# Optimization experiments

Measured on AMD Instinct MI355X. Metric: run time of the kernel, lower is better.

The kernel has to match this reference:

```python
import jax, jax.numpy as jnp
import numpy as np

V, E, H, O, B, T = 50000, 128, 128, 128, 64, 512


def setup_inputs() -> dict:
    key = jax.random.key(0)
    ks = jax.random.split(key, 16)
    s = 0.05
    X = jax.random.randint(ks[0], (B, T), 0, V)
    lens = jnp.sort(jax.random.randint(ks[1], (B,), 64, T + 1))[::-1]
    lens = lens.at[0].set(T)  # pack_padded needs descending lengths, max == T
    emb = jax.random.normal(ks[2], (V, E)) * s
    emb = emb.at[0].set(0.0)  # padding_idx = 0
    return {
        "X": X,
        "X_lengths": lens,
        "batch_size": B,
        "emb": emb,
        "W_e2i": jax.random.normal(ks[3], (H, E)) * s,
        "b_e2i": jax.random.normal(ks[4], (H,)) * s,
        "Wih_f": jax.random.normal(ks[5], (3 * H, H)) * s,
        "Whh_f": jax.random.normal(ks[6], (3 * H, H)) * s,
        "bih_f": jax.random.normal(ks[7], (3 * H,)) * s,
        "bhh_f": jax.random.normal(ks[8], (3 * H,)) * s,
        "Wih_b": jax.random.normal(ks[9], (3 * H, H)) * s,
        "Whh_b": jax.random.normal(ks[10], (3 * H, H)) * s,
        "bih_b": jax.random.normal(ks[11], (3 * H,)) * s,
        "bhh_b": jax.random.normal(ks[12], (3 * H,)) * s,
        "W_h2o": jax.random.normal(ks[13], (O, 2 * H)) * s,
        "b_h2o": jax.random.normal(ks[14], (O,)) * s,
        "u_w": jax.random.uniform(ks[15], (O,)),  # torch.rand
    }


def _gru_scan(gx, mask_tb, Whh, bhh):
    """gx: [T,B,3H] precomputed input gates; mask_tb: [T,B,1] valid-step mask.
    Masked update emulates pack_padded_sequence: padded steps keep h unchanged
    (and h stays 0 before the first valid step of the reversed direction)."""
    h0 = jnp.zeros((gx.shape[1], Whh.shape[1]), gx.dtype)

    def step(h, tb):
        gxt, m = tb
        gh = h @ Whh.T + bhh
        gxr, gxz, gxn = jnp.split(gxt, 3, axis=-1)
        ghr, ghz, ghn = jnp.split(gh, 3, axis=-1)
        r = jax.nn.sigmoid(gxr + ghr)
        z = jax.nn.sigmoid(gxz + ghz)
        n = jnp.tanh(gxn + r * ghn)
        h_new = (1.0 - z) * n + z * h
        h = jnp.where(m, h_new, h)
        return h, h

    _, hs = jax.lax.scan(step, h0, (gx, mask_tb))
    return hs  # [T,B,H]


def reference(X, X_lengths, batch_size, emb, W_e2i, b_e2i,
              Wih_f, Whh_f, bih_f, bhh_f, Wih_b, Whh_b, bih_b, bhh_b,
              W_h2o, b_h2o, u_w):
    x = emb[X]                              # [B,T,E]
    x = x @ W_e2i.T + b_e2i                 # [B,T,H]
    Tn = x.shape[1]
    mask = jnp.arange(Tn)[None, :] < X_lengths[:, None]  # [B,T]
    m_tb = mask.T[:, :, None]               # [T,B,1]

    gx_f = (x @ Wih_f.T + bih_f).transpose(1, 0, 2)       # [T,B,3H]
    h_f = _gru_scan(gx_f, m_tb, Whh_f, bhh_f)             # [T,B,H]
    gx_b = (x @ Wih_b.T + bih_b).transpose(1, 0, 2)[::-1]
    h_b = _gru_scan(gx_b, m_tb[::-1], Whh_b, bhh_b)[::-1]

    Hout = jnp.concatenate([h_f, h_b], axis=-1).transpose(1, 0, 2)  # [B,T,2H]
    Hout = Hout * mask[:, :, None].astype(Hout.dtype)  # pad_packed zeros pads

    Y = jnp.tanh(Hout @ W_h2o.T + b_h2o)               # [B,T,O]
    scores = jnp.where(mask, (Y * u_w).sum(-1), -jnp.inf)  # [B,T]
    alpha = jax.nn.softmax(scores, axis=1)             # per-sample softmax over valid steps
    pooled = jnp.einsum("bt,btd->bd", alpha, Hout)     # [B,2H]
    return pooled[None]                                # [1,B,2H]
```

## Files before the change

kernel.cpp:

```cpp
#include <hip/hip_runtime.h>
#include <hip/hip_bf16.h>

#define VV 50000
#define EE 128
#define HH 128
#define OO 128
#define BB 64
#define TT 512

typedef __bf16 bf16_t;
typedef __attribute__((ext_vector_type(8))) __bf16 bf16x8;
typedef __attribute__((ext_vector_type(4))) __bf16 bf16x4;
typedef __attribute__((ext_vector_type(4))) float floatx4;

__device__ __forceinline__ bf16x8 ldb8(const bf16_t* p) {
    return *reinterpret_cast<const bf16x8*>(p);
}

__device__ __forceinline__ bf16x8 ldf8_bf(const float* p) {
    const float4* q = reinterpret_cast<const float4*>(p);
    float4 u = q[0], v = q[1];
    bf16x8 r;
    r[0] = (__bf16)u.x; r[1] = (__bf16)u.y; r[2] = (__bf16)u.z; r[3] = (__bf16)u.w;
    r[4] = (__bf16)v.x; r[5] = (__bf16)v.y; r[6] = (__bf16)v.z; r[7] = (__bf16)v.w;
    return r;
}

__device__ __forceinline__ float fast_rcp(float x) { return __builtin_amdgcn_rcpf(x); }
__device__ __forceinline__ float sigmoid_f(float x) {
    return fast_rcp(1.0f + __expf(-x));
}
__device__ __forceinline__ float tanh_f(float x) {
    float e = __expf(2.0f * x);
    return 1.0f - 2.0f * fast_rcp(e + 1.0f);
}

__device__ __forceinline__ void lds_barrier() {
    asm volatile("s_waitcnt lgkmcnt(0)\n\ts_barrier" ::: "memory");
}

__global__ __launch_bounds__(256) void k0_conv(
    const float* __restrict__ we,
    const float* __restrict__ wihf, const float* __restrict__ wihb,
    const float* __restrict__ whhf, const float* __restrict__ whhb,
    const float* __restrict__ wh2o,
    const float* __restrict__ bihf, const float* __restrict__ bhhf,
    const float* __restrict__ bihb, const float* __restrict__ bhhb,
    bf16_t* __restrict__ we_bf,
    bf16_t* __restrict__ wih_bf, bf16_t* __restrict__ whh_bf,
    bf16_t* __restrict__ wh2o_bf, float* __restrict__ gxbias) {
    int tid = blockIdx.x * 256 + threadIdx.x;
    int np = gridDim.x * 256;
    for (int i = tid; i < HH * EE; i += np) we_bf[i] = (bf16_t)we[i];
    for (int i = tid; i < 384 * HH; i += np) {
        wih_bf[i] = (bf16_t)wihf[i];
        wih_bf[384 * HH + i] = (bf16_t)wihb[i];
        whh_bf[i] = (bf16_t)whhf[i];
        whh_bf[384 * HH + i] = (bf16_t)whhb[i];
    }
    for (int i = tid; i < OO * 256; i += np) wh2o_bf[i] = (bf16_t)wh2o[i];
    if (tid < 768) {
        int dir = tid / 384, n = tid % 384;
        const float* bih = dir ? bihb : bihf;
        const float* bhh = dir ? bhhb : bhhf;
        gxbias[tid] = bih[n] + (n < 256 ? bhh[n] : 0.0f);
    }
}

__global__ __launch_bounds__(256) void k12_gx(const int* __restrict__ X,
                                              const float* __restrict__ emb,
                                              const bf16_t* __restrict__ we_bf,
                                              const float* __restrict__ be,
                                              const bf16_t* __restrict__ wih_bf,
                                              const float* __restrict__ gxbias,
                                              const int* __restrict__ lens,
                                              bf16_t* __restrict__ gx3) {
    int blk = blockIdx.x;
    int tq = blk >> 2;
    int g = blk & 3;
    if (4 * tq >= lens[16 * g]) return;

    int lane = threadIdx.x & 63;
    int w2 = threadIdx.x >> 6;
    int quad = lane >> 4, col = lane & 15;

    __shared__ bf16_t xs[4][16 * 136];

#pragma unroll
    for (int tt = 0; tt < 4; ++tt) {
        int t = 4 * tq + tt;
        int v = X[(g * 16 + col) * TT + t];
        bf16x8 a[4];
#pragma unroll
        for (int kc = 0; kc < 4; ++kc)
            a[kc] = ldf8_bf(emb + (size_t)v * EE + kc * 32 + quad * 8);
#pragma unroll
        for (int tl = 0; tl < 2; ++tl) {
            int n = 32 * w2 + 16 * tl + col;
            floatx4 acc = {0.f, 0.f, 0.f, 0.f};
#pragma unroll
            for (int kc = 0; kc < 4; ++kc) {
                bf16x8 bw = ldb8(we_bf + (size_t)n * EE + kc * 32 + quad * 8);
                acc = __builtin_amdgcn_mfma_f32_16x16x32_bf16(a[kc], bw, acc, 0, 0, 0);
            }
            float bias = be[n];
#pragma unroll
            for (int r = 0; r < 4; ++r)
                xs[tt][(quad * 4 + r) * 136 + n] = (bf16_t)(acc[r] + bias);
        }
    }
    __syncthreads();

    bf16x8 a2[4][4];
#pragma unroll
    for (int tt = 0; tt < 4; ++tt)
#pragma unroll
        for (int kc = 0; kc < 4; ++kc)
            a2[tt][kc] = ldb8(xs[tt] + col * 136 + kc * 32 + quad * 8);

#pragma unroll
    for (int tl = 0; tl < 12; ++tl) {
        int idx = w2 * 12 + tl;
        int dir = idx >= 24;
        int n = (idx - dir * 24) * 16 + col;
        bf16x8 bw[4];
#pragma unroll
        for (int kc = 0; kc < 4; ++kc)
            bw[kc] = ldb8(wih_bf + ((size_t)dir * 384 + n) * HH + kc * 32 + quad * 8);
        float bias = gxbias[dir * 384 + n];
#pragma unroll
        for (int tt = 0; tt < 4; ++tt) {
            int t = 4 * tq + tt;
            floatx4 acc = {0.f, 0.f, 0.f, 0.f};
#pragma unroll
            for (int kc = 0; kc < 4; ++kc)
                acc = __builtin_amdgcn_mfma_f32_16x16x32_bf16(a2[tt][kc], bw[kc], acc, 0, 0, 0);
            bf16x4 pack;
#pragma unroll
            for (int r = 0; r < 4; ++r)
                pack[r] = (__bf16)(acc[r] + bias);
            *reinterpret_cast<bf16x4*>(
                gx3 + (((size_t)(dir * 16 + 4 * g + quad) * TT + t) * 384 + n) * 4) = pack;
        }
    }
}

#define HPAD 144
#define HBUF (4 * HPAD)
__global__ __launch_bounds__(512) void k3_gru(const bf16_t* __restrict__ gx3,
                                              const bf16_t* __restrict__ whh_bf,
                                              const float* __restrict__ bhh_f,
                                              const float* __restrict__ bhh_b,
                                              const int* __restrict__ lens,
                                              bf16_t* __restrict__ hist2) {
    int g16 = blockIdx.x;
    int dir = blockIdx.y;
    const float* bhh = dir ? bhh_b : bhh_f;

    int tid = threadIdx.x;
    int w = tid >> 6;
    int lane = tid & 63;
    int quad = lane >> 4, col = lane & 15;
    int j = 16 * w + col;

    __shared__ bf16_t hl[2 * HBUF];
    for (int i = tid; i < 2 * HBUF; i += 512) hl[i] = (bf16_t)0.f;

    int len1 = lens[4 * g16 + quad];
    int Lmax = max(max(lens[4 * g16], lens[4 * g16 + 1]),
                   max(lens[4 * g16 + 2], lens[4 * g16 + 3]));

    float bhn = bhh[256 + j];

    bf16x8 Bw[3][4];
#pragma unroll
    for (int gate = 0; gate < 3; ++gate)
#pragma unroll
        for (int kc = 0; kc < 4; ++kc)
            Bw[gate][kc] = ldb8(whh_bf + ((size_t)dir * 384 + gate * 128 + j) * HH + kc * 32 + quad * 8);

    const bf16_t* gbase = gx3 + (size_t)(dir * 16 + g16) * TT * 1536;
    bf16_t* hb = hist2 + (size_t)(dir * 16 + g16) * TT * 512;
    int loff[3];
#pragma unroll
    for (int gate = 0; gate < 3; ++gate)
        loff[gate] = (gate * 128 + j) * 4 + quad;
    int hoff = quad * 128 + j;
    int aoff = (col & 3) * HPAD + quad * 8;

    float h = 0.f;
    int S4 = (Lmax + 3) & ~3;
    bool lowquad = (quad & 1) == 0;
    bool lowhalf = (quad & 2) == 0;

    __bf16 ring[4][3];
#pragma unroll
    for (int u = 0; u < 4; ++u) {
        int tr = dir ? (Lmax - 1 - u) : u;
        int t = min(max(tr, 0), Lmax - 1);
#pragma unroll
        for (int gate = 0; gate < 3; ++gate)
            ring[u][gate] = gbase[(size_t)t * 1536 + loff[gate]];
    }
    lds_barrier();

    for (int sb = 0; sb < S4; sb += 4) {
#pragma unroll
        for (int u = 0; u < 4; ++u) {
            int s = sb + u;
            int tr = dir ? (Lmax - 1 - s) : s;
            int t = min(max(tr, 0), Lmax - 1);
            const bf16_t* hc = hl + (s & 1) * HBUF;
            bf16_t* hn = hl + ((s + 1) & 1) * HBUF;

            float gx0 = (float)ring[u][0];
            float gx1 = (float)ring[u][1];
            float gx2 = (float)ring[u][2];

            bf16x8 a[4];
#pragma unroll
            for (int kc = 0; kc < 4; ++kc)
                a[kc] = ldb8(hc + aoff + kc * 32);

            floatx4 cr = {0.f, 0.f, 0.f, 0.f};
            floatx4 cz = {0.f, 0.f, 0.f, 0.f};
            floatx4 cn = {bhn, bhn, bhn, bhn};
#pragma unroll
            for (int kc = 0; kc < 4; ++kc) {
                cr = __builtin_amdgcn_mfma_f32_16x16x32_bf16(a[kc], Bw[0][kc], cr, 0, 0, 0);
                cz = __builtin_amdgcn_mfma_f32_16x16x32_bf16(a[kc], Bw[1][kc], cz, 0, 0, 0);
                cn = __builtin_amdgcn_mfma_f32_16x16x32_bf16(a[kc], Bw[2][kc], cn, 0, 0, 0);
            }

            {
                int sn = s + 4;
                int trn = dir ? (Lmax - 1 - sn) : sn;
                int tn = min(max(trn, 0), Lmax - 1);
#pragma unroll
                for (int gate = 0; gate < 3; ++gate)
                    ring[u][gate] = gbase[(size_t)tn * 1536 + loff[gate]];
            }

            float aR = lowhalf ? (lowquad ? cr[0] : cr[1]) : (lowquad ? cr[2] : cr[3]);
            float aZ = lowhalf ? (lowquad ? cz[0] : cz[1]) : (lowquad ? cz[2] : cz[3]);
            float aN = lowhalf ? (lowquad ? cn[0] : cn[1]) : (lowquad ? cn[2] : cn[3]);

            float rg = sigmoid_f(aR + gx0);
            float zg = sigmoid_f(aZ + gx1);
            float ng = tanh_f(gx2 + rg * aN);
            float hnew = ng + zg * (h - ng);
            bool upd = (s < Lmax) && (t < len1);
            h = upd ? hnew : h;
            bf16_t h16 = (bf16_t)h;
            hn[quad * HPAD + j] = h16;
            hb[(size_t)t * 512 + hoff] = h16;

            lds_barrier();
        }
    }
}

__global__ __launch_bounds__(256) void k45_pool(const bf16_t* __restrict__ hist2,
                                                const bf16_t* __restrict__ wh2o_bf,
                                                const float* __restrict__ bh2o,
                                                const float* __restrict__ uw,
                                                const int* __restrict__ lens,
                                                float* __restrict__ out) {
    int b = blockIdx.x;
    int g16 = b >> 2, bl = b & 3;
    int tid = threadIdx.x;
    int lane = tid & 63, w2 = tid >> 6;
    int quad = lane >> 4, col = lane & 15;
    int len = lens[b];

    __shared__ float smax[TT][4];
    __shared__ float alpha[TT];
    __shared__ float red[256];

    const bf16_t* hf = hist2 + (size_t)g16 * TT * 512 + bl * 128;
    const bf16_t* hbk = hist2 + (size_t)(16 + g16) * TT * 512 + bl * 128;

    int n0 = (w2 * 2 + 0) * 16 + col;
    int n1 = (w2 * 2 + 1) * 16 + col;
    float bias0 = bh2o[n0], u0 = uw[n0];
    float bias1 = bh2o[n1], u1 = uw[n1];

    int nch = (len + 15) >> 4;
    for (int ch = 0; ch < nch; ++ch) {
        int t0 = ch * 16;
        int t = t0 + col;
        bf16x8 a[8];
#pragma unroll
        for (int kc = 0; kc < 4; ++kc) {
            a[kc]     = ldb8(hf  + (size_t)t * 512 + kc * 32 + quad * 8);
            a[kc + 4] = ldb8(hbk + (size_t)t * 512 + kc * 32 + quad * 8);
        }
        float p4[4] = {0.f, 0.f, 0.f, 0.f};
#pragma unroll
        for (int tl = 0; tl < 2; ++tl) {
            int n = tl ? n1 : n0;
            float bias = tl ? bias1 : bias0;
            float u = tl ? u1 : u0;
            floatx4 acc = {0.f, 0.f, 0.f, 0.f};
#pragma unroll
            for (int kc = 0; kc < 8; ++kc) {
                bf16x8 bw = ldb8(wh2o_bf + (size_t)n * 256 + kc * 32 + quad * 8);
                acc = __builtin_amdgcn_mfma_f32_16x16x32_bf16(a[kc], bw, acc, 0, 0, 0);
            }
#pragma unroll
            for (int r = 0; r < 4; ++r)
                p4[r] += tanh_f(acc[r] + bias) * u;
        }
#pragma unroll
        for (int m = 1; m < 16; m <<= 1)
#pragma unroll
            for (int r = 0; r < 4; ++r)
                p4[r] += __shfl_xor(p4[r], m, 64);
        if (col == 0) {
#pragma unroll
            for (int r = 0; r < 4; ++r)
                smax[t0 + quad * 4 + r][w2] = p4[r];
        }
    }
    __syncthreads();

    float mx = -1e30f;
    for (int t = tid; t < TT; t += 256) {
        float s = -1e30f;
        if (t < len) s = smax[t][0] + smax[t][1] + smax[t][2] + smax[t][3];
        alpha[t] = s;
        mx = fmaxf(mx, s);
    }
    red[tid] = mx;
    __syncthreads();
    for (int s = 128; s > 0; s >>= 1) {
        if (tid < s) red[tid] = fmaxf(red[tid], red[tid + s]);
        __syncthreads();
    }
    mx = red[0];
    __syncthreads();
    float sum = 0.f;
    for (int t = tid; t < TT; t += 256) {
        float e = (t < len) ? __expf(alpha[t] - mx) : 0.f;
        alpha[t] = e;
        sum += e;
    }
    red[tid] = sum;
    __syncthreads();
    for (int s = 128; s > 0; s >>= 1) {
        if (tid < s) red[tid] += red[tid + s];
        __syncthreads();
    }
    float inv = fast_rcp(red[0]);
    __syncthreads();

    int c = tid;
    int dir = c >> 7;
    int j = c & 127;
    const bf16_t* hbase = (dir ? hbk : hf) + j;
    float acc = 0.f;
    int t = 0;
    for (; t + 4 <= len; t += 4) {
        acc += alpha[t + 0] * (float)hbase[(size_t)(t + 0) * 512];
        acc += alpha[t + 1] * (float)hbase[(size_t)(t + 1) * 512];
        acc += alpha[t + 2] * (float)hbase[(size_t)(t + 2) * 512];
        acc += alpha[t + 3] * (float)hbase[(size_t)(t + 3) * 512];
    }
    for (; t < len; ++t) acc += alpha[t] * (float)hbase[(size_t)t * 512];

    out[(size_t)b * 256 + c] = acc * inv;
}

extern "C" void kernel_launch(void* const* d_in, const int* in_sizes, int n_in,
                              void* d_out, int out_size, void* d_ws, size_t ws_size,
                              hipStream_t stream) {
    const int* X       = (const int*)d_in[0];
    const int* lens    = (const int*)d_in[1];
    const float* emb   = (const float*)d_in[3];
    const float* We2i  = (const float*)d_in[4];
    const float* be2i  = (const float*)d_in[5];
    const float* Wihf  = (const float*)d_in[6];
    const float* Whhf  = (const float*)d_in[7];
    const float* bihf  = (const float*)d_in[8];
    const float* bhhf  = (const float*)d_in[9];
    const float* Wihb  = (const float*)d_in[10];
    const float* Whhb  = (const float*)d_in[11];
    const float* bihb  = (const float*)d_in[12];
    const float* bhhb  = (const float*)d_in[13];
    const float* Wh2o  = (const float*)d_in[14];
    const float* bh2o  = (const float*)d_in[15];
    const float* uw    = (const float*)d_in[16];

    char* ws = (char*)d_ws;
    size_t off = 0;
    bf16_t* we_bf = (bf16_t*)(ws + off);   off += (size_t)HH * EE * 2;
    bf16_t* wih_bf = (bf16_t*)(ws + off);  off += (size_t)2 * 384 * HH * 2;
    bf16_t* whh_bf = (bf16_t*)(ws + off);  off += (size_t)2 * 384 * HH * 2;
    bf16_t* wh2o_bf = (bf16_t*)(ws + off); off += (size_t)OO * 256 * 2;
    float* gxbias = (float*)(ws + off);    off += 768 * 4;
    off = (off + 255) & ~(size_t)255;
    bf16_t* gx3 = (bf16_t*)(ws + off);     off += (size_t)32 * TT * 384 * 4 * 2;
    bf16_t* hist2 = (bf16_t*)(ws + off);   off += (size_t)32 * TT * 4 * 128 * 2;

    float* out = (float*)d_out;

    k0_conv<<<dim3(256), dim3(256), 0, stream>>>(We2i, Wihf, Wihb, Whhf, Whhb,
                                                 Wh2o, bihf, bhhf, bihb, bhhb,
                                                 we_bf, wih_bf, whh_bf, wh2o_bf, gxbias);
    k12_gx<<<dim3(TT), dim3(256), 0, stream>>>(X, emb, we_bf, be2i, wih_bf, gxbias, lens, gx3);
    k3_gru<<<dim3(16, 2), dim3(512), 0, stream>>>(gx3, whh_bf, bhhf, bhhb, lens, hist2);
    k45_pool<<<dim3(BB), dim3(256), 0, stream>>>(hist2, wh2o_bf, bh2o, uw, lens, out);
}
```

Before: 395.6 us.

## Halve GRU block to 4 waves, each computing two hidden-column tiles with split-K accumulators

The recurrent GRU kernel now runs 256 threads instead of 512, and each wave covers two 16-column tiles of the hidden state, so it holds twice the recurrent weights in registers. The K reduction is split into two independent accumulator chains that are summed afterwards, which shortens the dependent MFMA chain. The aim is a cheaper per-step barrier across fewer waves and more instruction-level parallelism per wave. In exchange, each wave does twice the serial work per step and uses more registers.

```diff
diff --git a/kernel.cpp b/kernel.cpp
--- a/kernel.cpp
+++ b/kernel.cpp
@@ -37,6 +37,10 @@
 
 __device__ __forceinline__ void lds_barrier() {
     asm volatile("s_waitcnt lgkmcnt(0)\n\ts_barrier" ::: "memory");
+}
+
+__device__ __forceinline__ float sel4(floatx4 v, bool lowquad, bool lowhalf) {
+    return lowhalf ? (lowquad ? v[0] : v[1]) : (lowquad ? v[2] : v[3]);
 }
 
 __global__ __launch_bounds__(256) void k0_conv(
@@ -147,12 +151,12 @@
 
 #define HPAD 144
 #define HBUF (4 * HPAD)
-__global__ __launch_bounds__(512) void k3_gru(const bf16_t* __restrict__ gx3,
-                                              const bf16_t* __restrict__ whh_bf,
-                                              const float* __restrict__ bhh_f,
-                                              const float* __restrict__ bhh_b,
-                                              const int* __restrict__ lens,
-                                              bf16_t* __restrict__ hist2) {
+__global__ __launch_bounds__(256, 1) void k3_gru(const bf16_t* __restrict__ gx3,
+                                                 const bf16_t* __restrict__ whh_bf,
+                                                 const float* __restrict__ bhh_f,
+                                                 const float* __restrict__ bhh_b,
+                                                 const int* __restrict__ lens,
+                                                 bf16_t* __restrict__ hist2) {
     int g16 = blockIdx.x;
     int dir = blockIdx.y;
     const float* bhh = dir ? bhh_b : bhh_f;
@@ -161,46 +165,55 @@
     int w = tid >> 6;
     int lane = tid & 63;
     int quad = lane >> 4, col = lane & 15;
-    int j = 16 * w + col;
+    int j0 = 16 * w + col;
+    int j1 = j0 + 64;
 
     __shared__ bf16_t hl[2 * HBUF];
-    for (int i = tid; i < 2 * HBUF; i += 512) hl[i] = (bf16_t)0.f;
+    for (int i = tid; i < 2 * HBUF; i += 256) hl[i] = (bf16_t)0.f;
 
     int len1 = lens[4 * g16 + quad];
     int Lmax = max(max(lens[4 * g16], lens[4 * g16 + 1]),
                    max(lens[4 * g16 + 2], lens[4 * g16 + 3]));
 
-    float bhn = bhh[256 + j];
-
-    bf16x8 Bw[3][4];
-#pragma unroll
-    for (int gate = 0; gate < 3; ++gate)
-#pragma unroll
-        for (int kc = 0; kc < 4; ++kc)
-            Bw[gate][kc] = ldb8(whh_bf + ((size_t)dir * 384 + gate * 128 + j) * HH + kc * 32 + quad * 8);
+    float bhn0 = bhh[256 + j0];
+    float bhn1 = bhh[256 + j1];
+
+    bf16x8 Bw[2][3][4];
+#pragma unroll
+    for (int c = 0; c < 2; ++c)
+#pragma unroll
+        for (int gate = 0; gate < 3; ++gate)
+#pragma unroll
+            for (int kc = 0; kc < 4; ++kc)
+                Bw[c][gate][kc] = ldb8(whh_bf + ((size_t)dir * 384 + gate * 128 + (c ? j1 : j0)) * HH
+                                        + kc * 32 + quad * 8);
 
     const bf16_t* gbase = gx3 + (size_t)(dir * 16 + g16) * TT * 1536;
     bf16_t* hb = hist2 + (size_t)(dir * 16 + g16) * TT * 512;
-    int loff[3];
-#pragma unroll
-    for (int gate = 0; gate < 3; ++gate)
-        loff[gate] = (gate * 128 + j) * 4 + quad;
-    int hoff = quad * 128 + j;
+    int loff[6];
+#pragma unroll
+    for (int c = 0; c < 2; ++c)
+#pragma unroll
+        for (int gate = 0; gate < 3; ++gate)
+            loff[c * 3 + gate] = (gate * 128 + (c ? j1 : j0)) * 4 + quad;
+    int hoff0 = quad * 128 + j0;
+    int hoff1 = quad * 128 + j1;
     int aoff = (col & 3) * HPAD + quad * 8;
 
-    float h = 0.f;
+    float h0 = 0.f, h1 = 0.f;
     int S4 = (Lmax + 3) & ~3;
     bool lowquad = (quad & 1) == 0;
     bool lowhalf = (quad & 2) == 0;
 
-    __bf16 ring[4][3];
+    __bf16 ring[4][6];
 #pragma unroll
     for (int u = 0; u < 4; ++u) {
         int tr = dir ? (Lmax - 1 - u) : u;
         int t = min(max(tr, 0), Lmax - 1);
-#pragma unroll
-        for (int gate = 0; gate < 3; ++gate)
-            ring[u][gate] = gbase[(size_t)t * 1536 + loff[gate]];
+        size_t tb = (size_t)t * 1536;
+#pragma unroll
+        for (int q = 0; q < 6; ++q)
+            ring[u][q] = gbase[tb + loff[q]];
     }
     lds_barrier();
 
@@ -213,47 +226,82 @@
             const bf16_t* hc = hl + (s & 1) * HBUF;
             bf16_t* hn = hl + ((s + 1) & 1) * HBUF;
 
-            float gx0 = (float)ring[u][0];
-            float gx1 = (float)ring[u][1];
-            float gx2 = (float)ring[u][2];
+            float gx00 = (float)ring[u][0];
+            float gx01 = (float)ring[u][1];
+            float gx02 = (float)ring[u][2];
+            float gx10 = (float)ring[u][3];
+            float gx11 = (float)ring[u][4];
+            float gx12 = (float)ring[u][5];
 
             bf16x8 a[4];
 #pragma unroll
             for (int kc = 0; kc < 4; ++kc)
                 a[kc] = ldb8(hc + aoff + kc * 32);
 
-            floatx4 cr = {0.f, 0.f, 0.f, 0.f};
-            floatx4 cz = {0.f, 0.f, 0.f, 0.f};
-            floatx4 cn = {bhn, bhn, bhn, bhn};
-#pragma unroll
-            for (int kc = 0; kc < 4; ++kc) {
-                cr = __builtin_amdgcn_mfma_f32_16x16x32_bf16(a[kc], Bw[0][kc], cr, 0, 0, 0);
-                cz = __builtin_amdgcn_mfma_f32_16x16x32_bf16(a[kc], Bw[1][kc], cz, 0, 0, 0);
-                cn = __builtin_amdgcn_mfma_f32_16x16x32_bf16(a[kc], Bw[2][kc], cn, 0, 0, 0);
+            floatx4 crA[2], crB[2], czA[2], czB[2], cnA[2], cnB[2];
+#pragma unroll
+            for (int c = 0; c < 2; ++c) {
+                crA[c] = (floatx4){0.f, 0.f, 0.f, 0.f};
+                crB[c] = (floatx4){0.f, 0.f, 0.f, 0.f};
+                czA[c] = (floatx4){0.f, 0.f, 0.f, 0.f};
+                czB[c] = (floatx4){0.f, 0.f, 0.f, 0.f};
+                float bh = c ? bhn1 : bhn0;
+                cnA[c] = (floatx4){bh, bh, bh, bh};
+                cnB[c] = (floatx4){0.f, 0.f, 0.f, 0.f};
             }
+#pragma unroll
+            for (int kc = 0; kc < 2; ++kc)
+#pragma unroll
+                for (int c = 0; c < 2; ++c) {
+                    crA[c] = __builtin_amdgcn_mfma_f32_16x16x32_bf16(a[kc], Bw[c][0][kc], crA[c], 0, 0, 0);
+                    czA[c] = __builtin_amdgcn_mfma_f32_16x16x32_bf16(a[kc], Bw[c][1][kc], czA[c], 0, 0, 0);
+                    cnA[c] = __builtin_amdgcn_mfma_f32_16x16x32_bf16(a[kc], Bw[c][2][kc], cnA[c], 0, 0, 0);
+                }
+#pragma unroll
+            for (int kc = 2; kc < 4; ++kc)
+#pragma unroll
+                for (int c = 0; c < 2; ++c) {
+                    crB[c] = __builtin_amdgcn_mfma_f32_16x16x32_bf16(a[kc], Bw[c][0][kc], crB[c], 0, 0, 0);
+                    czB[c] = __builtin_amdgcn_mfma_f32_16x16x32_bf16(a[kc], Bw[c][1][kc], czB[c], 0, 0, 0);
+                    cnB[c] = __builtin_amdgcn_mfma_f32_16x16x32_bf16(a[kc], Bw[c][2][kc], cnB[c], 0, 0, 0);
+                }
 
             {
                 int sn = s + 4;
                 int trn = dir ? (Lmax - 1 - sn) : sn;
                 int tn = min(max(trn, 0), Lmax - 1);
-#pragma unroll
-                for (int gate = 0; gate < 3; ++gate)
-                    ring[u][gate] = gbase[(size_t)tn * 1536 + loff[gate]];
+                size_t tb = (size_t)tn * 1536;
+#pragma unroll
+                for (int q = 0; q < 6; ++q)
+                    ring[u][q] = gbase[tb + loff[q]];
             }
 
-            float aR = lowhalf ? (lowquad ? cr[0] : cr[1]) : (lowquad ? cr[2] : cr[3]);
-            float aZ = lowhalf ? (lowquad ? cz[0] : cz[1]) : (lowquad ? cz[2] : cz[3]);
-            float aN = lowhalf ? (lowquad ? cn[0] : cn[1]) : (lowquad ? cn[2] : cn[3]);
-
-            float rg = sigmoid_f(aR + gx0);
-            float zg = sigmoid_f(aZ + gx1);
-            float ng = tanh_f(gx2 + rg * aN);
-            float hnew = ng + zg * (h - ng);
             bool upd = (s < Lmax) && (t < len1);
-            h = upd ? hnew : h;
-            bf16_t h16 = (bf16_t)h;
-            hn[quad * HPAD + j] = h16;
-            hb[(size_t)t * 512 + hoff] = h16;
+
+            float aR0 = sel4(crA[0], lowquad, lowhalf) + sel4(crB[0], lowquad, lowhalf);
+            float aZ0 = sel4(czA[0], lowquad, lowhalf) + sel4(czB[0], lowquad, lowhalf);
+            float aN0 = sel4(cnA[0], lowquad, lowhalf) + sel4(cnB[0], lowquad, lowhalf);
+            float rg0 = sigmoid_f(aR0 + gx00);
+            float zg0 = sigmoid_f(aZ0 + gx01);
+            float ng0 = tanh_f(gx02 + rg0 * aN0);
+            float hnew0 = ng0 + zg0 * (h0 - ng0);
+            h0 = upd ? hnew0 : h0;
+
+            float aR1 = sel4(crA[1], lowquad, lowhalf) + sel4(crB[1], lowquad, lowhalf);
+            float aZ1 = sel4(czA[1], lowquad, lowhalf) + sel4(czB[1], lowquad, lowhalf);
+            float aN1 = sel4(cnA[1], lowquad, lowhalf) + sel4(cnB[1], lowquad, lowhalf);
+            float rg1 = sigmoid_f(aR1 + gx10);
+            float zg1 = sigmoid_f(aZ1 + gx11);
+            float ng1 = tanh_f(gx12 + rg1 * aN1);
+            float hnew1 = ng1 + zg1 * (h1 - ng1);
+            h1 = upd ? hnew1 : h1;
+
+            bf16_t h16a = (bf16_t)h0;
+            bf16_t h16b = (bf16_t)h1;
+            hn[quad * HPAD + j0] = h16a;
+            hn[quad * HPAD + j1] = h16b;
+            hb[(size_t)t * 512 + hoff0] = h16a;
+            hb[(size_t)t * 512 + hoff1] = h16b;
 
             lds_barrier();
         }
@@ -408,6 +456,6 @@
                                                  Wh2o, bihf, bhhf, bihb, bhhb,
                                                  we_bf, wih_bf, whh_bf, wh2o_bf, gxbias);
     k12_gx<<<dim3(TT), dim3(256), 0, stream>>>(X, emb, we_bf, be2i, wih_bf, gxbias, lens, gx3);
-    k3_gru<<<dim3(16, 2), dim3(512), 0, stream>>>(gx3, whh_bf, bhhf, bhhb, lens, hist2);
+    k3_gru<<<dim3(16, 2), dim3(256), 0, stream>>>(gx3, whh_bf, bhhf, bhhb, lens, hist2);
     k45_pool<<<dim3(BB), dim3(256), 0, stream>>>(hist2, wh2o_bf, bh2o, uw, lens, out);
 }
```

New measurement: 477.8 us. 20.8% more time.

## Prescale GRU gate weights for exp2 activations, replicate A rows, vectorize pooling

Applied to the files above, without the earlier changes.

Folds the -log2(e) and 2*log2(e) factors into the converted W_ih/W_hh weights and biases, so the recurrent step can use raw exp2 and fused multiply-adds instead of expf-based sigmoid/tanh. The A-operand row mapping changes so every accumulator element holds the same batch row, which removes the per-lane selects over cr/cz/cn. The pooling stage switches from scalar strided loads to 8-wide bf16 vector loads split across 8 time slices, followed by a shared-memory reduction. Applying the scale before bf16 rounding slightly changes the quantised weights, and the pooling reduction reuses the smax shared buffer, which must be large enough.

```diff
diff --git a/kernel.cpp b/kernel.cpp
--- a/kernel.cpp
+++ b/kernel.cpp
@@ -12,6 +12,9 @@
 typedef __attribute__((ext_vector_type(8))) __bf16 bf16x8;
 typedef __attribute__((ext_vector_type(4))) __bf16 bf16x4;
 typedef __attribute__((ext_vector_type(4))) float floatx4;
+
+#define SC_RZ (-1.4426950408889634f)
+#define SC_N  (2.8853900817779268f)
 
 __device__ __forceinline__ bf16x8 ldb8(const bf16_t* p) {
     return *reinterpret_cast<const bf16x8*>(p);
@@ -27,9 +30,7 @@
 }
 
 __device__ __forceinline__ float fast_rcp(float x) { return __builtin_amdgcn_rcpf(x); }
-__device__ __forceinline__ float sigmoid_f(float x) {
-    return fast_rcp(1.0f + __expf(-x));
-}
+__device__ __forceinline__ float exp2_f(float x) { return __builtin_amdgcn_exp2f(x); }
 __device__ __forceinline__ float tanh_f(float x) {
     float e = __expf(2.0f * x);
     return 1.0f - 2.0f * fast_rcp(e + 1.0f);
@@ -53,17 +54,20 @@
     int np = gridDim.x * 256;
     for (int i = tid; i < HH * EE; i += np) we_bf[i] = (bf16_t)we[i];
     for (int i = tid; i < 384 * HH; i += np) {
-        wih_bf[i] = (bf16_t)wihf[i];
-        wih_bf[384 * HH + i] = (bf16_t)wihb[i];
-        whh_bf[i] = (bf16_t)whhf[i];
-        whh_bf[384 * HH + i] = (bf16_t)whhb[i];
+        int nrow = i >> 7;
+        float sc = (nrow < 256) ? SC_RZ : SC_N;
+        wih_bf[i] = (bf16_t)(sc * wihf[i]);
+        wih_bf[384 * HH + i] = (bf16_t)(sc * wihb[i]);
+        whh_bf[i] = (bf16_t)(sc * whhf[i]);
+        whh_bf[384 * HH + i] = (bf16_t)(sc * whhb[i]);
     }
     for (int i = tid; i < OO * 256; i += np) wh2o_bf[i] = (bf16_t)wh2o[i];
     if (tid < 768) {
         int dir = tid / 384, n = tid % 384;
         const float* bih = dir ? bihb : bihf;
         const float* bhh = dir ? bhhb : bhhf;
-        gxbias[tid] = bih[n] + (n < 256 ? bhh[n] : 0.0f);
+        float sc = (n < 256) ? SC_RZ : SC_N;
+        gxbias[tid] = sc * bih[n] + (n < 256 ? sc * bhh[n] : 0.0f);
     }
 }
 
@@ -170,7 +174,7 @@
     int Lmax = max(max(lens[4 * g16], lens[4 * g16 + 1]),
                    max(lens[4 * g16 + 2], lens[4 * g16 + 3]));
 
-    float bhn = bhh[256 + j];
+    float bhn = SC_N * bhh[256 + j];
 
     bf16x8 Bw[3][4];
 #pragma unroll
@@ -186,12 +190,10 @@
     for (int gate = 0; gate < 3; ++gate)
         loff[gate] = (gate * 128 + j) * 4 + quad;
     int hoff = quad * 128 + j;
-    int aoff = (col & 3) * HPAD + quad * 8;
+    int aoff = (col >> 2) * HPAD + quad * 8;
 
     float h = 0.f;
     int S4 = (Lmax + 3) & ~3;
-    bool lowquad = (quad & 1) == 0;
-    bool lowhalf = (quad & 2) == 0;
 
     __bf16 ring[4][3];
 #pragma unroll
@@ -241,14 +243,12 @@
                     ring[u][gate] = gbase[(size_t)tn * 1536 + loff[gate]];
             }
 
-            float aR = lowhalf ? (lowquad ? cr[0] : cr[1]) : (lowquad ? cr[2] : cr[3]);
-            float aZ = lowhalf ? (lowquad ? cz[0] : cz[1]) : (lowquad ? cz[2] : cz[3]);
-            float aN = lowhalf ? (lowquad ? cn[0] : cn[1]) : (lowquad ? cn[2] : cn[3]);
-
-            float rg = sigmoid_f(aR + gx0);
-            float zg = sigmoid_f(aZ + gx1);
-            float ng = tanh_f(gx2 + rg * aN);
-            float hnew = ng + zg * (h - ng);
+            float rg = fast_rcp(1.0f + exp2_f(cr[0] + gx0));
+            float zg = fast_rcp(1.0f + exp2_f(cz[0] + gx1));
+            float v  = fmaf(rg, cn[0], gx2);
+            float ng = fmaf(-2.0f, fast_rcp(exp2_f(v) + 1.0f), 1.0f);
+            float hnew = fmaf(zg, h - ng, ng);
+
             bool upd = (s < Lmax) && (t < len1);
             h = upd ? hnew : h;
             bf16_t h16 = (bf16_t)h;
@@ -354,21 +354,32 @@
     float inv = fast_rcp(red[0]);
     __syncthreads();
 
-    int c = tid;
-    int dir = c >> 7;
-    int j = c & 127;
-    const bf16_t* hbase = (dir ? hbk : hf) + j;
-    float acc = 0.f;
-    int t = 0;
-    for (; t + 4 <= len; t += 4) {
-        acc += alpha[t + 0] * (float)hbase[(size_t)(t + 0) * 512];
-        acc += alpha[t + 1] * (float)hbase[(size_t)(t + 1) * 512];
-        acc += alpha[t + 2] * (float)hbase[(size_t)(t + 2) * 512];
-        acc += alpha[t + 3] * (float)hbase[(size_t)(t + 3) * 512];
-    }
-    for (; t < len; ++t) acc += alpha[t] * (float)hbase[(size_t)t * 512];
-
-    out[(size_t)b * 256 + c] = acc * inv;
+    {
+        int ts = tid >> 5, o = tid & 31;
+        int dirp = o >> 4;
+        int j8 = (o & 15) * 8;
+        const bf16_t* hbase = (dirp ? hbk : hf) + j8;
+        float acc8[8];
+#pragma unroll
+        for (int e = 0; e < 8; ++e) acc8[e] = 0.f;
+        for (int t = ts; t < len; t += 8) {
+            float al = alpha[t];
+            bf16x8 hv = ldb8(hbase + (size_t)t * 512);
+#pragma unroll
+            for (int e = 0; e < 8; ++e) acc8[e] = fmaf(al, (float)hv[e], acc8[e]);
+        }
+        float* red2 = &smax[0][0];
+#pragma unroll
+        for (int e = 0; e < 8; ++e) red2[(ts * 32 + o) * 8 + e] = acc8[e];
+        __syncthreads();
+        int c = tid;
+        int dir2 = c >> 7, rem = c & 127;
+        int oo = dir2 * 16 + (rem >> 3), ee = c & 7;
+        float acc = 0.f;
+#pragma unroll
+        for (int q = 0; q < 8; ++q) acc += red2[(q * 32 + oo) * 8 + ee];
+        out[(size_t)b * 256 + c] = acc * inv;
+    }
 }
 
 extern "C" void kernel_launch(void* const* d_in, const int* in_sizes, int n_in,
```

Result: faster. 387.2 us (-2.1%).
